# Performance work log

Hardware: AMD Instinct MI355X
Metric: run time of the kernel (lower is better)

The kernel has to match this reference:

```python
import jax, jax.numpy as jnp
import numpy as np

N, E, F, T, C, HOR = 50000, 800000, 4, 12, 32, 12


def setup_inputs() -> dict:
    key = jax.random.key(0)
    ks = jax.random.split(key, 24)
    def rn(k, shape, s=0.1):
        return jax.random.normal(k, shape, jnp.float32) * s
    inp = {
        "x": jax.random.normal(ks[0], (N, F, T), jnp.float32),
        "edge_index": jax.random.randint(ks[1], (2, E), 0, N, dtype=jnp.int64),
        "edge_weight": jax.random.uniform(ks[2], (E,), jnp.float32),
        "attention": jax.random.uniform(ks[3], (T,), jnp.float32),
    }
    names = ["Wz", "bz", "Wlz", "blz", "Wr", "br", "Wlr", "blr", "Wh", "bh", "Wlh", "blh"]
    shapes = [(F, C), (C,), (2 * C, C), (C,), (F, C), (C,), (2 * C, C), (C,), (F, C), (C,), (2 * C, C), (C,)]
    for i, (n, s) in enumerate(zip(names, shapes)):
        inp[n] = rn(ks[4 + i], s)
    inp["Wout"] = rn(ks[20], (C, HOR))
    inp["bout"] = jnp.zeros((HOR,), jnp.float32)
    return inp


def reference(x, edge_index, edge_weight, attention,
              Wz, bz, Wlz, blz, Wr, br, Wlr, blr, Wh, bh, Wlh, blh,
              Wout, bout):
    n = x.shape[0]
    c = Wz.shape[1]
    row, col = edge_index[0], edge_index[1]

    # GCN normalization with self-loops (weight 1): A_hat = D^-1/2 (A+I) D^-1/2
    deg = jax.ops.segment_sum(edge_weight, col, num_segments=n) + 1.0
    dis = 1.0 / jnp.sqrt(deg)                      # deg >= 1 thanks to self-loop
    norm = dis[row] * edge_weight * dis[col]       # [E]
    self_norm = dis * dis                          # [N] self-loop coefficient

    def conv(xt, W, b):
        # xt: [N, F] -> [N, C]; sparse normalized aggregation over edge list
        xw = xt @ W
        agg = jax.ops.segment_sum(norm[:, None] * xw[row], col, num_segments=n)
        return agg + self_norm[:, None] * xw + b

    probs = jax.nn.softmax(attention)              # attention over periods
    H0 = jnp.zeros((n, c), x.dtype)                # A3TGCN passes H=None each period
    H_accum = jnp.zeros((n, c), x.dtype)
    for t in range(x.shape[2]):                    # fixed small period loop (as original)
        xt = x[:, :, t]
        Z = jax.nn.sigmoid(jnp.concatenate([conv(xt, Wz, bz), H0], axis=1) @ Wlz + blz)
        R = jax.nn.sigmoid(jnp.concatenate([conv(xt, Wr, br), H0], axis=1) @ Wlr + blr)
        Ht = jnp.tanh(jnp.concatenate([conv(xt, Wh, bh), H0 * R], axis=1) @ Wlh + blh)
        Hn = Z * H0 + (1.0 - Z) * Ht               # GRU update from zero state
        H_accum = H_accum + probs[t] * Hn

    h = jax.nn.relu(H_accum)
    return h @ Wout + bout
```

## Files before the change

### kernel.cpp

```cpp
#include <hip/hip_runtime.h>
#include <hip/hip_bf16.h>

#define NN 50000
#define NE 800000
#define FD 4
#define TD 12
#define CD 32
#define HD 12
#define FT 48
#define NBANK 8

#define OFF_HEAD   0
#define OFF_NEXT   400000
#define OFF_DIS    1200000
#define OFF_CST    1250000

#define INIT_BLKS ((NBANK * NN + 255) / 256)
__global__ void init_pre_kernel(int* __restrict__ head,
                                const float* __restrict__ Wz, const float* __restrict__ bz,
                                const float* __restrict__ Wlz, const float* __restrict__ blz,
                                const float* __restrict__ Wh, const float* __restrict__ bh,
                                const float* __restrict__ Wlh, const float* __restrict__ blh,
                                const float* __restrict__ attention,
                                float* __restrict__ cst) {
    int tid = threadIdx.x;
    if (blockIdx.x < INIT_BLKS) {
        int i = blockIdx.x * 256 + tid;
        if (i < NBANK * NN) head[i] = -1;
        return;
    }
    if (tid < 128) {
        int f = tid >> 5, c = tid & 31;
        float s = 0.f, s2 = 0.f;
        #pragma unroll
        for (int k = 0; k < 32; ++k) {
            s  += Wz[f*32 + k] * Wlz[k*32 + c];
            s2 += Wh[f*32 + k] * Wlh[k*32 + c];
        }
        cst[tid]       = s;
        cst[160 + tid] = s2;
    } else if (tid < 160) {
        int c = tid - 128;
        float s = blz[c], s2 = blh[c];
        #pragma unroll
        for (int k = 0; k < 32; ++k) {
            s  += bz[k] * Wlz[k*32 + c];
            s2 += bh[k] * Wlh[k*32 + c];
        }
        cst[128 + c] = s;
        cst[288 + c] = s2;
    } else if (tid == 160) {
        float m = -1e30f;
        for (int t = 0; t < TD; ++t) m = fmaxf(m, attention[t]);
        float e[TD], s = 0.f;
        #pragma unroll
        for (int t = 0; t < TD; ++t) { e[t] = __expf(attention[t] - m); s += e[t]; }
        float inv = 1.f / s;
        #pragma unroll
        for (int t = 0; t < TD; ++t) cst[320 + t] = e[t] * inv;
    }
}

__global__ void build_kernel(const int* __restrict__ ei, int* __restrict__ head,
                             int* __restrict__ next) {
    int e = blockIdx.x * blockDim.x + threadIdx.x;
    if (e < NE) {
        int c = ei[NE + e];
        int old = atomicExch(&head[(e & (NBANK-1)) * NN + c], e);
        next[e] = old;
    }
}

__global__ void degdis_kernel(const int* __restrict__ head, const int* __restrict__ next,
                              const float* __restrict__ w, float* __restrict__ dis) {
    int t = blockIdx.x * blockDim.x + threadIdx.x;
    int i = t >> 3;
    int b = t & 7;
    if (i >= NN) return;
    float s = 0.f;
    int e = head[b * NN + i];
    while (e >= 0) { s += w[e]; e = next[e]; }
    s += __shfl_xor(s, 1, 8);
    s += __shfl_xor(s, 2, 8);
    s += __shfl_xor(s, 4, 8);
    if (b == 0) dis[i] = rsqrtf(s + 1.0f);
}

__global__ __launch_bounds__(256) void gather_gru_kernel(
        const float4* __restrict__ x4, const float* __restrict__ dis,
        const int* __restrict__ head, const int* __restrict__ next,
        const int* __restrict__ ei, const float* __restrict__ w,
        const float* __restrict__ cst, const float* __restrict__ Wout,
        const float* __restrict__ bout, float* __restrict__ out) {
    __shared__ float sy[16][FT];
    __shared__ float hbuf[16][CD];
    __shared__ float sAz[128], sAh[128], sCz[32], sCh[32], sP[TD];
    __shared__ float sWout[CD * HD], sBout[HD];

    int tid = threadIdx.x;
    if (tid < 128) { sAz[tid] = cst[tid]; sAh[tid] = cst[160 + tid]; }
    if (tid < 32)  { sCz[tid] = cst[128 + tid]; sCh[tid] = cst[288 + tid]; }
    if (tid < TD)  { sP[tid] = cst[320 + tid]; sBout[tid] = bout[tid]; }
    for (int k = tid; k < CD * HD; k += 256) sWout[k] = Wout[k];

    int lane = tid & 63;
    int g    = tid & 15;
    int ln   = tid >> 4;
    int i    = blockIdx.x * 16 + ln;

    float d = dis[i];
    int e = (g < 8) ? head[g * NN + i] : -1;
    float4 acc = make_float4(0.f, 0.f, 0.f, 0.f);

    unsigned long long bal = __ballot(e >= 0);
    unsigned int act = (unsigned int)((bal >> (lane & 48)) & 0xFFFFu);
    while (act) {
        int r = -1; float nv = 0.f; int nxt = -1;
        if (e >= 0) {
            r   = ei[e];
            nv  = dis[r] * w[e];
            nxt = next[e];
        }
        #pragma unroll
        for (int b = 0; b < NBANK; ++b) {
            int src  = (lane & 48) + b;
            int rb   = __shfl(r, src, 64);
            float nb = __shfl(nv, src, 64);
            if (rb >= 0 && g < 12) {
                float4 v = x4[rb * (FT/4) + g];
                acc.x += nb * v.x; acc.y += nb * v.y;
                acc.z += nb * v.z; acc.w += nb * v.w;
            }
        }
        e = nxt;
        bal = __ballot(e >= 0);
        act = (unsigned int)((bal >> (lane & 48)) & 0xFFFFu);
    }

    if (g < 12) {
        float4 a = x4[i * (FT/4) + g];
        float s0 = d * d;
        sy[ln][g*4 + 0] = a.x * s0 + d * acc.x;
        sy[ln][g*4 + 1] = a.y * s0 + d * acc.y;
        sy[ln][g*4 + 2] = a.z * s0 + d * acc.z;
        sy[ln][g*4 + 3] = a.w * s0 + d * acc.w;
    }
    __syncthreads();

    {
        int c0 = g, c1 = g + 16;
        float az00 = sAz[c0], az01 = sAz[32+c0], az02 = sAz[64+c0], az03 = sAz[96+c0];
        float az10 = sAz[c1], az11 = sAz[32+c1], az12 = sAz[64+c1], az13 = sAz[96+c1];
        float ah00 = sAh[c0], ah01 = sAh[32+c0], ah02 = sAh[64+c0], ah03 = sAh[96+c0];
        float ah10 = sAh[c1], ah11 = sAh[32+c1], ah12 = sAh[64+c1], ah13 = sAh[96+c1];
        float cz0 = sCz[c0], cz1 = sCz[c1], ch0 = sCh[c0], ch1 = sCh[c1];

        float hacc0 = 0.f, hacc1 = 0.f;
        #pragma unroll
        for (int t = 0; t < TD; ++t) {
            float y0 = sy[ln][0*TD + t];
            float y1 = sy[ln][1*TD + t];
            float y2 = sy[ln][2*TD + t];
            float y3 = sy[ln][3*TD + t];
            float z0 = cz0 + y0*az00 + y1*az01 + y2*az02 + y3*az03;
            float z1 = cz1 + y0*az10 + y1*az11 + y2*az12 + y3*az13;
            float h0 = ch0 + y0*ah00 + y1*ah01 + y2*ah02 + y3*ah03;
            float h1 = ch1 + y0*ah10 + y1*ah11 + y2*ah12 + y3*ah13;
            float Z0 = 1.f / (1.f + __expf(-z0));
            float Z1 = 1.f / (1.f + __expf(-z1));
            float e0 = __expf(2.f * h0);
            float e1 = __expf(2.f * h1);
            float H0v = (e0 - 1.f) / (e0 + 1.f);
            float H1v = (e1 - 1.f) / (e1 + 1.f);
            float p = sP[t];
            hacc0 += p * (1.f - Z0) * H0v;
            hacc1 += p * (1.f - Z1) * H1v;
        }
        hbuf[ln][c0] = fmaxf(hacc0, 0.f);
        hbuf[ln][c1] = fmaxf(hacc1, 0.f);
    }
    __syncthreads();

    if (tid < 16 * HD) {
        int lnode = tid / HD, hor = tid - lnode * HD;
        int gn = blockIdx.x * 16 + lnode;
        float s = sBout[hor];
        #pragma unroll
        for (int k = 0; k < CD; ++k) s += hbuf[lnode][k] * sWout[k * HD + hor];
        out[gn * HD + hor] = s;
    }
}

extern "C" void kernel_launch(void* const* d_in, const int* in_sizes, int n_in,
                              void* d_out, int out_size, void* d_ws, size_t ws_size,
                              hipStream_t stream) {
    const float* x      = (const float*)d_in[0];
    const int*   ei     = (const int*)d_in[1];
    const float* ew     = (const float*)d_in[2];
    const float* attn   = (const float*)d_in[3];
    const float* Wz     = (const float*)d_in[4];
    const float* bz     = (const float*)d_in[5];
    const float* Wlz    = (const float*)d_in[6];
    const float* blz    = (const float*)d_in[7];
    const float* Wh     = (const float*)d_in[12];
    const float* bh     = (const float*)d_in[13];
    const float* Wlh    = (const float*)d_in[14];
    const float* blh    = (const float*)d_in[15];
    const float* Wout   = (const float*)d_in[16];
    const float* bout   = (const float*)d_in[17];
    float* out = (float*)d_out;

    float* ws   = (float*)d_ws;
    int*   head = (int*)(ws + OFF_HEAD);
    int*   next = (int*)(ws + OFF_NEXT);
    float* dis  = ws + OFF_DIS;
    float* cst  = ws + OFF_CST;

    init_pre_kernel<<<INIT_BLKS + 1, 256, 0, stream>>>(head, Wz, bz, Wlz, blz,
                                                       Wh, bh, Wlh, blh, attn, cst);

    build_kernel<<<(NE + 255) / 256, 256, 0, stream>>>(ei, head, next);

    degdis_kernel<<<(NN * 8 + 255) / 256, 256, 0, stream>>>(head, next, ew, dis);

    gather_gru_kernel<<<NN / 16, 256, 0, stream>>>(
        (const float4*)x, dis, head, next, ei, ew, cst, Wout, bout, out);
}
```

Baseline: 234.5 us.

## Batch linked-list traversal into shared metadata and merge build with precompute

The gather kernel now has each bank-lane walk up to 8 list entries per round. A 16-lane prefix sum packs the (source, norm) pairs into a shared buffer, and all feature lanes then stream those neighbours with an unrolled loop. This replaces the per-step ballot and shuffle loop, exposing more independent loads and cutting wasted iterations when bank lists have uneven lengths. The head initialisation moves to hipMemsetAsync and the edge build is fused with the constant precompute kernel, which removes one launch. The self-feature load is also hoisted before the loop.

```diff
diff --git a/kernel.cpp b/kernel.cpp
--- a/kernel.cpp
+++ b/kernel.cpp
@@ -15,18 +15,20 @@
 #define OFF_DIS    1200000
 #define OFF_CST    1250000
 
-#define INIT_BLKS ((NBANK * NN + 255) / 256)
-__global__ void init_pre_kernel(int* __restrict__ head,
-                                const float* __restrict__ Wz, const float* __restrict__ bz,
-                                const float* __restrict__ Wlz, const float* __restrict__ blz,
-                                const float* __restrict__ Wh, const float* __restrict__ bh,
-                                const float* __restrict__ Wlh, const float* __restrict__ blh,
-                                const float* __restrict__ attention,
-                                float* __restrict__ cst) {
+__global__ void build_pre_kernel(const int* __restrict__ ei, int* __restrict__ head,
+                                 int* __restrict__ next,
+                                 const float* __restrict__ Wz, const float* __restrict__ bz,
+                                 const float* __restrict__ Wlz, const float* __restrict__ blz,
+                                 const float* __restrict__ Wh, const float* __restrict__ bh,
+                                 const float* __restrict__ Wlh, const float* __restrict__ blh,
+                                 const float* __restrict__ attention,
+                                 float* __restrict__ cst) {
     int tid = threadIdx.x;
-    if (blockIdx.x < INIT_BLKS) {
-        int i = blockIdx.x * 256 + tid;
-        if (i < NBANK * NN) head[i] = -1;
+    if (blockIdx.x < (NE / 256)) {
+        int e = blockIdx.x * 256 + tid;
+        int c = ei[NE + e];
+        int old = atomicExch(&head[(e & (NBANK-1)) * NN + c], e);
+        next[e] = old;
         return;
     }
     if (tid < 128) {
@@ -58,16 +60,6 @@
         float inv = 1.f / s;
         #pragma unroll
         for (int t = 0; t < TD; ++t) cst[320 + t] = e[t] * inv;
-    }
-}
-
-__global__ void build_kernel(const int* __restrict__ ei, int* __restrict__ head,
-                             int* __restrict__ next) {
-    int e = blockIdx.x * blockDim.x + threadIdx.x;
-    if (e < NE) {
-        int c = ei[NE + e];
-        int old = atomicExch(&head[(e & (NBANK-1)) * NN + c], e);
-        next[e] = old;
     }
 }
 
@@ -92,6 +84,7 @@
         const int* __restrict__ ei, const float* __restrict__ w,
         const float* __restrict__ cst, const float* __restrict__ Wout,
         const float* __restrict__ bout, float* __restrict__ out) {
+    __shared__ int2  smeta[16][64];
     __shared__ float sy[16][FT];
     __shared__ float hbuf[16][CD];
     __shared__ float sAz[128], sAh[128], sCz[32], sCh[32], sP[TD];
@@ -102,43 +95,60 @@
     if (tid < 32)  { sCz[tid] = cst[128 + tid]; sCh[tid] = cst[288 + tid]; }
     if (tid < TD)  { sP[tid] = cst[320 + tid]; sBout[tid] = bout[tid]; }
     for (int k = tid; k < CD * HD; k += 256) sWout[k] = Wout[k];
-
-    int lane = tid & 63;
-    int g    = tid & 15;
-    int ln   = tid >> 4;
-    int i    = blockIdx.x * 16 + ln;
+    __syncthreads();
+
+    int g  = tid & 15;
+    int ln = tid >> 4;
+    int i  = blockIdx.x * 16 + ln;
 
     float d = dis[i];
+    float4 a = (g < 12) ? x4[i * (FT/4) + g] : make_float4(0.f,0.f,0.f,0.f);
+    float4 acc = make_float4(0.f, 0.f, 0.f, 0.f);
+
     int e = (g < 8) ? head[g * NN + i] : -1;
-    float4 acc = make_float4(0.f, 0.f, 0.f, 0.f);
-
-    unsigned long long bal = __ballot(e >= 0);
-    unsigned int act = (unsigned int)((bal >> (lane & 48)) & 0xFFFFu);
-    while (act) {
-        int r = -1; float nv = 0.f; int nxt = -1;
-        if (e >= 0) {
-            r   = ei[e];
-            nv  = dis[r] * w[e];
-            nxt = next[e];
-        }
-        #pragma unroll
-        for (int b = 0; b < NBANK; ++b) {
-            int src  = (lane & 48) + b;
-            int rb   = __shfl(r, src, 64);
-            float nb = __shfl(nv, src, 64);
-            if (rb >= 0 && g < 12) {
-                float4 v = x4[rb * (FT/4) + g];
-                acc.x += nb * v.x; acc.y += nb * v.y;
-                acc.z += nb * v.z; acc.w += nb * v.w;
+
+    while (true) {
+        int r0=0,r1=0,r2=0,r3=0,r4=0,r5=0,r6=0,r7=0;
+        float n0=0,n1=0,n2=0,n3=0,n4=0,n5=0,n6=0,n7=0;
+        int cnt = 0;
+        #define STEP(RK,NK) if (e >= 0) { RK = ei[e]; NK = dis[RK] * w[e]; e = next[e]; ++cnt; }
+        STEP(r0,n0) STEP(r1,n1) STEP(r2,n2) STEP(r3,n3)
+        STEP(r4,n4) STEP(r5,n5) STEP(r6,n6) STEP(r7,n7)
+        #undef STEP
+
+        int incl = cnt;
+        #pragma unroll
+        for (int dd = 1; dd < 8; dd <<= 1) {
+            int t2 = __shfl_up(incl, dd, 16);
+            if (g >= dd) incl += t2;
+        }
+        int S = __shfl(incl, 7, 16);
+        if (S == 0) break;
+        int off = incl - cnt;
+
+        if (cnt > 0) smeta[ln][off + 0] = make_int2(r0, __float_as_int(n0));
+        if (cnt > 1) smeta[ln][off + 1] = make_int2(r1, __float_as_int(n1));
+        if (cnt > 2) smeta[ln][off + 2] = make_int2(r2, __float_as_int(n2));
+        if (cnt > 3) smeta[ln][off + 3] = make_int2(r3, __float_as_int(n3));
+        if (cnt > 4) smeta[ln][off + 4] = make_int2(r4, __float_as_int(n4));
+        if (cnt > 5) smeta[ln][off + 5] = make_int2(r5, __float_as_int(n5));
+        if (cnt > 6) smeta[ln][off + 6] = make_int2(r6, __float_as_int(n6));
+        if (cnt > 7) smeta[ln][off + 7] = make_int2(r7, __float_as_int(n7));
+        __builtin_amdgcn_wave_barrier();
+
+        if (g < 12) {
+            #pragma unroll 4
+            for (int k = 0; k < S; ++k) {
+                int2 m = smeta[ln][k];
+                float nv = __int_as_float(m.y);
+                float4 v = x4[m.x * (FT/4) + g];
+                acc.x += nv * v.x; acc.y += nv * v.y;
+                acc.z += nv * v.z; acc.w += nv * v.w;
             }
         }
-        e = nxt;
-        bal = __ballot(e >= 0);
-        act = (unsigned int)((bal >> (lane & 48)) & 0xFFFFu);
     }
 
     if (g < 12) {
-        float4 a = x4[i * (FT/4) + g];
         float s0 = d * d;
         sy[ln][g*4 + 0] = a.x * s0 + d * acc.x;
         sy[ln][g*4 + 1] = a.y * s0 + d * acc.y;
@@ -216,10 +226,11 @@
     float* dis  = ws + OFF_DIS;
     float* cst  = ws + OFF_CST;
 
-    init_pre_kernel<<<INIT_BLKS + 1, 256, 0, stream>>>(head, Wz, bz, Wlz, blz,
+    hipMemsetAsync(head, 0xFF, NBANK * NN * sizeof(int), stream);
+
+    build_pre_kernel<<<NE / 256 + 1, 256, 0, stream>>>(ei, head, next,
+                                                       Wz, bz, Wlz, blz,
                                                        Wh, bh, Wlh, blh, attn, cst);
-
-    build_kernel<<<(NE + 255) / 256, 256, 0, stream>>>(ei, head, next);
 
     degdis_kernel<<<(NN * 8 + 255) / 256, 256, 0, stream>>>(head, next, ew, dis);
 
```

Result: faster. 212.8 us (-9.3%).
